# Kernel tuning notes

Hardware: AMD Instinct MI355X
Metric: run time of the kernel (lower is better)

The kernel has to match this reference:

```python
import jax, jax.numpy as jnp
import numpy as np

ACTION_SCALE = 0.01
LOG_STD_MIN, LOG_STD_MAX = -20.0, 2.0


def setup_inputs() -> dict:
    key = jax.random.key(0)
    k1, k2, k3 = jax.random.split(key, 3)
    B, N, D = 8, 1024, 128
    kv = jax.random.normal(k1, (B, N, 4 * D), dtype=jnp.float32)
    positions = jax.random.normal(k2, (B, N, 3), dtype=jnp.float32)
    eps = jax.random.normal(k3, (B, N, 3), dtype=jnp.float32)  # standard-normal sample for rsample
    return {"kv": kv, "positions": positions, "eps": eps}


def reference(kv, positions, eps):
    # Split Atomwise output into mean/std key-value embeddings: each [B, N, D]
    k_mu, v_mu, k_sigma, v_sigma = jnp.split(kv, 4, axis=-1)

    # Low-rank attention-like pairwise scores: [B, N, N]
    rel_shifts_mean = jnp.einsum("bid,bjd->bij", k_mu, v_mu)
    rel_shifts_log_std = jnp.einsum("bid,bjd->bij", k_sigma, v_sigma)

    # All-pairs unit displacement vectors: [B, N, N, 3]
    P = positions[:, :, None, :] - positions[:, None, :, :]
    norm = jnp.linalg.norm(P, axis=-1) + 1e-8
    P = P / norm[..., None]

    # Weighted sum over the j axis (torch dim=-2): [B, N, 3]
    actions_mean = jnp.einsum("bijc,bij->bic", P, rel_shifts_mean)
    actions_log_std = jnp.clip(
        jnp.einsum("bijc,bij->bic", P, rel_shifts_log_std), LOG_STD_MIN, LOG_STD_MAX
    )
    actions_std = jnp.exp(actions_log_std)

    # TanhNormal rsample (training branch) with externally supplied noise eps
    pre_tanh = actions_mean + actions_std * eps
    actions = jnp.tanh(pre_tanh)

    # Normal log-prob minus tanh log-det-Jacobian
    normal_lp = (
        -0.5 * ((pre_tanh - actions_mean) / actions_std) ** 2
        - actions_log_std
        - 0.5 * jnp.log(2.0 * jnp.pi)
    )
    log_det = (
        2.0 * jnp.log(2.0)
        + jax.nn.log_sigmoid(2.0 * pre_tanh)
        + jax.nn.log_sigmoid(-2.0 * pre_tanh)
    )
    log_prob = jnp.sum(normal_lp - log_det, axis=(1, 2))[:, None]  # [B, 1]

    actions = actions * ACTION_SCALE
    # change-of-variables correction for the action_scale factor
    n_dims = pre_tanh.shape[1] * pre_tanh.shape[2]
    log_prob = log_prob - n_dims * jnp.log(ACTION_SCALE)
    return actions, log_prob
```

## Files before the change

### kernel.cpp

```cpp
#include <hip/hip_runtime.h>
#include <math.h>


#define NTOK 1024
#define LPCONST 14147.0828114f

typedef __bf16 bf16x8 __attribute__((ext_vector_type(8)));
typedef float f32x4 __attribute__((ext_vector_type(4)));
#define MFMA(a, b, c) __builtin_amdgcn_mfma_f32_16x16x32_bf16(a, b, c, 0, 0, 0)

__device__ __forceinline__ unsigned short to_bf16(float x) {
    return (unsigned short)((__float_as_uint(x) + 0x8000u) >> 16);
}

template <int CTRL>
__device__ __forceinline__ float dpp_add(float v) {
    int y = __builtin_amdgcn_update_dpp(0, __float_as_int(v), CTRL, 0xf, 0xf, true);
    return v + __int_as_float(y);
}
__device__ __forceinline__ float red16(float v) {
    v = dpp_add<0xB1>(v);
    v = dpp_add<0x4E>(v);
    v = dpp_add<0x141>(v);
    v = dpp_add<0x140>(v);
    return v;
}

__global__ __launch_bounds__(256) void prepass_kernel(
    const float* __restrict__ kv, unsigned short* __restrict__ frag)
{
    const int t = blockIdx.x * 256 + threadIdx.x;
    const int lane = t & 63;
    const int kc   = (t >> 6) & 3;
    const int tile = (t >> 8) & 63;
    const int b    = (t >> 14) & 7;
    const int side = t >> 17;

    const int row = tile * 16 + (lane & 15);
    const int kof = kc * 32 + (lane >> 4) * 8;
    const float* gp = kv + ((size_t)b * NTOK + row) * 512 + side * 128 + kof;
    const float4 m0 = *(const float4*)gp;
    const float4 m1 = *(const float4*)(gp + 4);
    const float4 s0 = *(const float4*)(gp + 256);
    const float4 s1 = *(const float4*)(gp + 260);

    unsigned short* cp = frag + (size_t)side * 2097152 +
                         ((size_t)(((b * 64 + tile) * 4 + kc) * 2) << 9) + lane * 8;
    ushort4 h0, h1;
    h0.x = to_bf16(m0.x); h0.y = to_bf16(m0.y); h0.z = to_bf16(m0.z); h0.w = to_bf16(m0.w);
    h1.x = to_bf16(m1.x); h1.y = to_bf16(m1.y); h1.z = to_bf16(m1.z); h1.w = to_bf16(m1.w);
    *(ushort4*)(cp + 0) = h0; *(ushort4*)(cp + 4) = h1;
    h0.x = to_bf16(s0.x); h0.y = to_bf16(s0.y); h0.z = to_bf16(s0.z); h0.w = to_bf16(s0.w);
    h1.x = to_bf16(s1.x); h1.y = to_bf16(s1.y); h1.z = to_bf16(s1.z); h1.w = to_bf16(s1.w);
    *(ushort4*)(cp + 512) = h0; *(ushort4*)(cp + 516) = h1;
}

__global__ __launch_bounds__(256) void actor_gemm_kernel(
    const unsigned short* __restrict__ frag, const float* __restrict__ pos,
    float* __restrict__ partial, float* __restrict__ out)
{
    const int t = threadIdx.x;
    const int w = t >> 6;
    const int lane = t & 63;
    const int q = lane >> 4;
    const int r16 = lane & 15;
    const int js = blockIdx.x;
    const int itb = blockIdx.y;
    const int b = blockIdx.z;
    const int i0 = itb * 64;
    const int jb = js * 128;

    const unsigned short* fragA = frag;
    const unsigned short* fragB = frag + 2097152;
    const float* posb = pos + (size_t)b * NTOK * 3;

    const int atile0 = b * 64 + itb * 4;
    const int btile0 = b * 64 + js * 8 + w * 2;
    const int lofs = lane * 8;

    f32x4 accm[4][2], accs[4][2];
    #pragma unroll
    for (int ig = 0; ig < 4; ++ig)
        #pragma unroll
        for (int jg = 0; jg < 2; ++jg) {
            accm[ig][jg] = (f32x4){0.f, 0.f, 0.f, 0.f};
            accs[ig][jg] = (f32x4){0.f, 0.f, 0.f, 0.f};
        }

    #pragma unroll
    for (int kc = 0; kc < 4; ++kc) {
        bf16x8 Bm[2], Bs[2];
        #pragma unroll
        for (int jg = 0; jg < 2; ++jg) {
            const unsigned short* bp =
                fragB + (((size_t)(btile0 + jg) * 8 + kc * 2) << 9) + lofs;
            Bm[jg] = *(const bf16x8*)(bp);
            Bs[jg] = *(const bf16x8*)(bp + 512);
        }
        #pragma unroll
        for (int ig = 0; ig < 4; ++ig) {
            const unsigned short* ap =
                fragA + (((size_t)(atile0 + ig) * 8 + kc * 2) << 9) + lofs;
            const bf16x8 Am = *(const bf16x8*)(ap);
            const bf16x8 As = *(const bf16x8*)(ap + 512);
            #pragma unroll
            for (int jg = 0; jg < 2; ++jg) {
                accm[ig][jg] = MFMA(Am, Bm[jg], accm[ig][jg]);
                accs[ig][jg] = MFMA(As, Bs[jg], accs[ig][jg]);
            }
        }
    }

    float am[4][4][3] = {};
    float al[4][4][3] = {};
    float pj[2][3];
    #pragma unroll
    for (int jg = 0; jg < 2; ++jg) {
        const int j = jb + w * 32 + jg * 16 + r16;
        pj[jg][0] = posb[j * 3 + 0];
        pj[jg][1] = posb[j * 3 + 1];
        pj[jg][2] = posb[j * 3 + 2];
    }
    #pragma unroll
    for (int ig = 0; ig < 4; ++ig)
        #pragma unroll
        for (int reg = 0; reg < 4; ++reg) {
            const int i = i0 + ig * 16 + q * 4 + reg;
            const float pix = posb[i * 3 + 0];
            const float piy = posb[i * 3 + 1];
            const float piz = posb[i * 3 + 2];
            #pragma unroll
            for (int jg = 0; jg < 2; ++jg) {
                const float dx = pix - pj[jg][0];
                const float dy = piy - pj[jg][1];
                const float dz = piz - pj[jg][2];
                const float d2 = dx * dx + dy * dy + dz * dz;
                const float inv = d2 > 0.f ? rsqrtf(d2) : 0.f;
                const float wm = accm[ig][jg][reg] * inv;
                const float ws = accs[ig][jg][reg] * inv;
                am[ig][reg][0] = fmaf(dx, wm, am[ig][reg][0]);
                am[ig][reg][1] = fmaf(dy, wm, am[ig][reg][1]);
                am[ig][reg][2] = fmaf(dz, wm, am[ig][reg][2]);
                al[ig][reg][0] = fmaf(dx, ws, al[ig][reg][0]);
                al[ig][reg][1] = fmaf(dy, ws, al[ig][reg][1]);
                al[ig][reg][2] = fmaf(dz, ws, al[ig][reg][2]);
            }
        }

    #pragma unroll
    for (int ig = 0; ig < 4; ++ig)
        #pragma unroll
        for (int reg = 0; reg < 4; ++reg)
            #pragma unroll
            for (int c = 0; c < 3; ++c) {
                am[ig][reg][c] = red16(am[ig][reg][c]);
                al[ig][reg][c] = red16(al[ig][reg][c]);
            }

    __shared__ float wacc[4 * 64 * 6];
    if (r16 == 0) {
        #pragma unroll
        for (int ig = 0; ig < 4; ++ig)
            #pragma unroll
            for (int reg = 0; reg < 4; ++reg) {
                const int row = ig * 16 + q * 4 + reg;
                float* p = wacc + (w * 64 + row) * 6;
                p[0] = am[ig][reg][0]; p[1] = am[ig][reg][1]; p[2] = am[ig][reg][2];
                p[3] = al[ig][reg][0]; p[4] = al[ig][reg][1]; p[5] = al[ig][reg][2];
            }
    }
    __syncthreads();
    for (int u = t; u < 384; u += 256) {
        const int row = u / 6, c = u - row * 6;
        const float v = wacc[row * 6 + c] + wacc[(64 + row) * 6 + c] +
                        wacc[(128 + row) * 6 + c] + wacc[(192 + row) * 6 + c];
        partial[((size_t)((js * 8 + b) * NTOK) + i0 + row) * 6 + c] = v;
    }
    if (js == 0 && itb == 0 && t == 0) out[8 * NTOK * 3 + b] = LPCONST;
}

__device__ __forceinline__ float softplusf(float z) {
    return z > 20.f ? z : log1pf(expf(z));
}

__global__ __launch_bounds__(64) void actor_tail_kernel(
    const float* __restrict__ partial, const float* __restrict__ eps,
    float* __restrict__ out)
{
    const int b = blockIdx.x >> 4;
    const int i = (blockIdx.x & 15) * 64 + threadIdx.x;
    const int gi = b * NTOK + i;

    float am[3] = {}, al[3] = {};
    #pragma unroll
    for (int js = 0; js < 8; ++js) {
        const float* p = partial + (((size_t)js * 8 + b) * NTOK + i) * 6;
        const float2 v0 = *(const float2*)(p);
        const float2 v1 = *(const float2*)(p + 2);
        const float2 v2 = *(const float2*)(p + 4);
        am[0] += v0.x; am[1] += v0.y; am[2] += v1.x;
        al[0] += v1.y; al[1] += v2.x; al[2] += v2.y;
    }

    float lp = 0.f;
    #pragma unroll
    for (int c = 0; c < 3; ++c) {
        const float als = fminf(fmaxf(al[c], -20.f), 2.f);
        const float sd = expf(als);
        const float e = eps[gi * 3 + c];
        const float pre = fmaf(sd, e, am[c]);
        out[gi * 3 + c] = tanhf(pre) * 0.01f;
        const float t2 = 2.f * pre;
        lp += -0.5f * e * e - als - 2.3052328944f + softplusf(t2) + softplusf(-t2);
    }

    #pragma unroll
    for (int m = 1; m < 64; m <<= 1) lp += __shfl_xor(lp, m, 64);
    if (threadIdx.x == 0) atomicAdd(out + NTOK * 8 * 3 + b, lp);
}

extern "C" void kernel_launch(void* const* d_in, const int* in_sizes, int n_in,
                              void* d_out, int out_size, void* d_ws, size_t ws_size,
                              hipStream_t stream) {
    const float* kv = (const float*)d_in[0];
    const float* pos = (const float*)d_in[1];
    const float* eps = (const float*)d_in[2];
    float* out = (float*)d_out;
    float* partial = (float*)d_ws;
    unsigned short* frag = (unsigned short*)((char*)d_ws + (2 << 20));

    prepass_kernel<<<dim3(1024), 256, 0, stream>>>(kv, frag);
    actor_gemm_kernel<<<dim3(8, 16, 8), 256, 0, stream>>>(frag, pos, partial, out);
    actor_tail_kernel<<<dim3(128), 64, 0, stream>>>(partial, eps, out);
}
```

Baseline: 100.1 us.

## Fuse GEMM and tail into one kernel with full-row j sweep per block

Restructures the main kernel so each block owns 16 rows i and sweeps all 1024 j columns across its 4 waves. This removes the cross-block partial-sum buffer and lets the tail math (tanh, log-prob, atomic add) run in the same kernel, so the third launch goes away. The log-prob constant is now initialised in the prepass, and the fragment layout is simplified. The trade-off is fewer blocks (512), less register reuse of the A/B fragments per MFMA, and per-lane position loads inside the j loop.

```diff
diff --git a/kernel.cpp b/kernel.cpp
--- a/kernel.cpp
+++ b/kernel.cpp
@@ -26,10 +26,17 @@
     return v;
 }
 
+__device__ __forceinline__ float softplusf(float z) {
+    return z > 20.f ? z : log1pf(expf(z));
+}
+
 __global__ __launch_bounds__(256) void prepass_kernel(
-    const float* __restrict__ kv, unsigned short* __restrict__ frag)
+    const float* __restrict__ kv, unsigned short* __restrict__ frag,
+    float* __restrict__ out)
 {
     const int t = blockIdx.x * 256 + threadIdx.x;
+    if (t < 8) out[8 * NTOK * 3 + t] = LPCONST;
+
     const int lane = t & 63;
     const int kc   = (t >> 6) & 3;
     const int tile = (t >> 8) & 63;
@@ -45,7 +52,7 @@
     const float4 s1 = *(const float4*)(gp + 260);
 
     unsigned short* cp = frag + (size_t)side * 2097152 +
-                         ((size_t)(((b * 64 + tile) * 4 + kc) * 2) << 9) + lane * 8;
+                         (size_t)(b * 64 + tile) * 4096 + kc * 1024 + lane * 8;
     ushort4 h0, h1;
     h0.x = to_bf16(m0.x); h0.y = to_bf16(m0.y); h0.z = to_bf16(m0.z); h0.w = to_bf16(m0.w);
     h1.x = to_bf16(m1.x); h1.y = to_bf16(m1.y); h1.z = to_bf16(m1.z); h1.w = to_bf16(m1.w);
@@ -55,168 +62,104 @@
     *(ushort4*)(cp + 512) = h0; *(ushort4*)(cp + 516) = h1;
 }
 
-__global__ __launch_bounds__(256) void actor_gemm_kernel(
+__global__ __launch_bounds__(256) void actor_kernel(
     const unsigned short* __restrict__ frag, const float* __restrict__ pos,
-    float* __restrict__ partial, float* __restrict__ out)
+    const float* __restrict__ eps, float* __restrict__ out)
 {
     const int t = threadIdx.x;
     const int w = t >> 6;
     const int lane = t & 63;
     const int q = lane >> 4;
     const int r16 = lane & 15;
-    const int js = blockIdx.x;
-    const int itb = blockIdx.y;
-    const int b = blockIdx.z;
-    const int i0 = itb * 64;
-    const int jb = js * 128;
+    const int itx = blockIdx.x;
+    const int b = blockIdx.y;
+    const int i0 = itx * 16;
 
-    const unsigned short* fragA = frag;
-    const unsigned short* fragB = frag + 2097152;
+    const unsigned short* fragK = frag;
+    const unsigned short* fragV = frag + 2097152;
     const float* posb = pos + (size_t)b * NTOK * 3;
 
-    const int atile0 = b * 64 + itb * 4;
-    const int btile0 = b * 64 + js * 8 + w * 2;
-    const int lofs = lane * 8;
-
-    f32x4 accm[4][2], accs[4][2];
-    #pragma unroll
-    for (int ig = 0; ig < 4; ++ig)
-        #pragma unroll
-        for (int jg = 0; jg < 2; ++jg) {
-            accm[ig][jg] = (f32x4){0.f, 0.f, 0.f, 0.f};
-            accs[ig][jg] = (f32x4){0.f, 0.f, 0.f, 0.f};
-        }
-
+    const unsigned short* kp = fragK + (size_t)(b * 64 + itx) * 4096 + lane * 8;
+    bf16x8 Km[4], Ks[4];
     #pragma unroll
     for (int kc = 0; kc < 4; ++kc) {
-        bf16x8 Bm[2], Bs[2];
+        Km[kc] = *(const bf16x8*)(kp + kc * 1024);
+        Ks[kc] = *(const bf16x8*)(kp + kc * 1024 + 512);
+    }
+
+    const int i = i0 + r16;
+    const float pix = posb[i * 3 + 0];
+    const float piy = posb[i * 3 + 1];
+    const float piz = posb[i * 3 + 2];
+
+    float am0 = 0.f, am1 = 0.f, am2 = 0.f;
+    float al0 = 0.f, al1 = 0.f, al2 = 0.f;
+
+    const unsigned short* vbase =
+        fragV + (size_t)(b * 64 + w * 16) * 4096 + lane * 8;
+
+    #pragma unroll 2
+    for (int jt = 0; jt < 16; ++jt) {
+        const unsigned short* vp = vbase + jt * 4096;
+        f32x4 accm = (f32x4){0.f, 0.f, 0.f, 0.f};
+        f32x4 accs = (f32x4){0.f, 0.f, 0.f, 0.f};
         #pragma unroll
-        for (int jg = 0; jg < 2; ++jg) {
-            const unsigned short* bp =
-                fragB + (((size_t)(btile0 + jg) * 8 + kc * 2) << 9) + lofs;
-            Bm[jg] = *(const bf16x8*)(bp);
-            Bs[jg] = *(const bf16x8*)(bp + 512);
+        for (int kc = 0; kc < 4; ++kc) {
+            const bf16x8 Vm = *(const bf16x8*)(vp + kc * 1024);
+            const bf16x8 Vs = *(const bf16x8*)(vp + kc * 1024 + 512);
+            accm = MFMA(Vm, Km[kc], accm);
+            accs = MFMA(Vs, Ks[kc], accs);
         }
+        const int jbase = (w * 16 + jt) * 16 + q * 4;
         #pragma unroll
-        for (int ig = 0; ig < 4; ++ig) {
-            const unsigned short* ap =
-                fragA + (((size_t)(atile0 + ig) * 8 + kc * 2) << 9) + lofs;
-            const bf16x8 Am = *(const bf16x8*)(ap);
-            const bf16x8 As = *(const bf16x8*)(ap + 512);
-            #pragma unroll
-            for (int jg = 0; jg < 2; ++jg) {
-                accm[ig][jg] = MFMA(Am, Bm[jg], accm[ig][jg]);
-                accs[ig][jg] = MFMA(As, Bs[jg], accs[ig][jg]);
-            }
+        for (int reg = 0; reg < 4; ++reg) {
+            const float* pj = posb + (jbase + reg) * 3;
+            const float dx = pix - pj[0];
+            const float dy = piy - pj[1];
+            const float dz = piz - pj[2];
+            const float d2 = dx * dx + dy * dy + dz * dz;
+            const float inv = d2 > 0.f ? rsqrtf(d2) : 0.f;
+            const float wm = accm[reg] * inv;
+            const float ws = accs[reg] * inv;
+            am0 = fmaf(dx, wm, am0); am1 = fmaf(dy, wm, am1); am2 = fmaf(dz, wm, am2);
+            al0 = fmaf(dx, ws, al0); al1 = fmaf(dy, ws, al1); al2 = fmaf(dz, ws, al2);
         }
     }
 
-    float am[4][4][3] = {};
-    float al[4][4][3] = {};
-    float pj[2][3];
-    #pragma unroll
-    for (int jg = 0; jg < 2; ++jg) {
-        const int j = jb + w * 32 + jg * 16 + r16;
-        pj[jg][0] = posb[j * 3 + 0];
-        pj[jg][1] = posb[j * 3 + 1];
-        pj[jg][2] = posb[j * 3 + 2];
-    }
-    #pragma unroll
-    for (int ig = 0; ig < 4; ++ig)
-        #pragma unroll
-        for (int reg = 0; reg < 4; ++reg) {
-            const int i = i0 + ig * 16 + q * 4 + reg;
-            const float pix = posb[i * 3 + 0];
-            const float piy = posb[i * 3 + 1];
-            const float piz = posb[i * 3 + 2];
-            #pragma unroll
-            for (int jg = 0; jg < 2; ++jg) {
-                const float dx = pix - pj[jg][0];
-                const float dy = piy - pj[jg][1];
-                const float dz = piz - pj[jg][2];
-                const float d2 = dx * dx + dy * dy + dz * dz;
-                const float inv = d2 > 0.f ? rsqrtf(d2) : 0.f;
-                const float wm = accm[ig][jg][reg] * inv;
-                const float ws = accs[ig][jg][reg] * inv;
-                am[ig][reg][0] = fmaf(dx, wm, am[ig][reg][0]);
-                am[ig][reg][1] = fmaf(dy, wm, am[ig][reg][1]);
-                am[ig][reg][2] = fmaf(dz, wm, am[ig][reg][2]);
-                al[ig][reg][0] = fmaf(dx, ws, al[ig][reg][0]);
-                al[ig][reg][1] = fmaf(dy, ws, al[ig][reg][1]);
-                al[ig][reg][2] = fmaf(dz, ws, al[ig][reg][2]);
-            }
-        }
+    am0 += __shfl_xor(am0, 16, 64); am0 += __shfl_xor(am0, 32, 64);
+    am1 += __shfl_xor(am1, 16, 64); am1 += __shfl_xor(am1, 32, 64);
+    am2 += __shfl_xor(am2, 16, 64); am2 += __shfl_xor(am2, 32, 64);
+    al0 += __shfl_xor(al0, 16, 64); al0 += __shfl_xor(al0, 32, 64);
+    al1 += __shfl_xor(al1, 16, 64); al1 += __shfl_xor(al1, 32, 64);
+    al2 += __shfl_xor(al2, 16, 64); al2 += __shfl_xor(al2, 32, 64);
 
-    #pragma unroll
-    for (int ig = 0; ig < 4; ++ig)
-        #pragma unroll
-        for (int reg = 0; reg < 4; ++reg)
-            #pragma unroll
-            for (int c = 0; c < 3; ++c) {
-                am[ig][reg][c] = red16(am[ig][reg][c]);
-                al[ig][reg][c] = red16(al[ig][reg][c]);
-            }
-
-    __shared__ float wacc[4 * 64 * 6];
-    if (r16 == 0) {
-        #pragma unroll
-        for (int ig = 0; ig < 4; ++ig)
-            #pragma unroll
-            for (int reg = 0; reg < 4; ++reg) {
-                const int row = ig * 16 + q * 4 + reg;
-                float* p = wacc + (w * 64 + row) * 6;
-                p[0] = am[ig][reg][0]; p[1] = am[ig][reg][1]; p[2] = am[ig][reg][2];
-                p[3] = al[ig][reg][0]; p[4] = al[ig][reg][1]; p[5] = al[ig][reg][2];
-            }
+    __shared__ float wacc[4 * 16 * 6];
+    __shared__ float fin[16 * 6];
+    if (lane < 16) {
+        float* p = wacc + (w * 16 + r16) * 6;
+        p[0] = am0; p[1] = am1; p[2] = am2; p[3] = al0; p[4] = al1; p[5] = al2;
     }
     __syncthreads();
-    for (int u = t; u < 384; u += 256) {
-        const int row = u / 6, c = u - row * 6;
-        const float v = wacc[row * 6 + c] + wacc[(64 + row) * 6 + c] +
-                        wacc[(128 + row) * 6 + c] + wacc[(192 + row) * 6 + c];
-        partial[((size_t)((js * 8 + b) * NTOK) + i0 + row) * 6 + c] = v;
+    if (t < 96) fin[t] = wacc[t] + wacc[96 + t] + wacc[192 + t] + wacc[288 + t];
+    __syncthreads();
+
+    if (t < 16) {
+        const int gi = b * NTOK + i0 + t;
+        const float* v = fin + t * 6;
+        float lp = 0.f;
+        #pragma unroll
+        for (int c = 0; c < 3; ++c) {
+            const float als = fminf(fmaxf(v[3 + c], -20.f), 2.f);
+            const float sd = expf(als);
+            const float e = eps[gi * 3 + c];
+            const float pre = fmaf(sd, e, v[c]);
+            out[gi * 3 + c] = tanhf(pre) * 0.01f;
+            const float t2 = 2.f * pre;
+            lp += -0.5f * e * e - als - 2.3052328944f + softplusf(t2) + softplusf(-t2);
+        }
+        lp = red16(lp);
+        if (t == 0) atomicAdd(out + 8 * NTOK * 3 + b, lp);
     }
-    if (js == 0 && itb == 0 && t == 0) out[8 * NTOK * 3 + b] = LPCONST;
-}
-
-__device__ __forceinline__ float softplusf(float z) {
-    return z > 20.f ? z : log1pf(expf(z));
-}
-
-__global__ __launch_bounds__(64) void actor_tail_kernel(
-    const float* __restrict__ partial, const float* __restrict__ eps,
-    float* __restrict__ out)
-{
-    const int b = blockIdx.x >> 4;
-    const int i = (blockIdx.x & 15) * 64 + threadIdx.x;
-    const int gi = b * NTOK + i;
-
-    float am[3] = {}, al[3] = {};
-    #pragma unroll
-    for (int js = 0; js < 8; ++js) {
-        const float* p = partial + (((size_t)js * 8 + b) * NTOK + i) * 6;
-        const float2 v0 = *(const float2*)(p);
-        const float2 v1 = *(const float2*)(p + 2);
-        const float2 v2 = *(const float2*)(p + 4);
-        am[0] += v0.x; am[1] += v0.y; am[2] += v1.x;
-        al[0] += v1.y; al[1] += v2.x; al[2] += v2.y;
-    }
-
-    float lp = 0.f;
-    #pragma unroll
-    for (int c = 0; c < 3; ++c) {
-        const float als = fminf(fmaxf(al[c], -20.f), 2.f);
-        const float sd = expf(als);
-        const float e = eps[gi * 3 + c];
-        const float pre = fmaf(sd, e, am[c]);
-        out[gi * 3 + c] = tanhf(pre) * 0.01f;
-        const float t2 = 2.f * pre;
-        lp += -0.5f * e * e - als - 2.3052328944f + softplusf(t2) + softplusf(-t2);
-    }
-
-    #pragma unroll
-    for (int m = 1; m < 64; m <<= 1) lp += __shfl_xor(lp, m, 64);
-    if (threadIdx.x == 0) atomicAdd(out + NTOK * 8 * 3 + b, lp);
 }
 
 extern "C" void kernel_launch(void* const* d_in, const int* in_sizes, int n_in,
@@ -226,10 +169,8 @@
     const float* pos = (const float*)d_in[1];
     const float* eps = (const float*)d_in[2];
     float* out = (float*)d_out;
-    float* partial = (float*)d_ws;
-    unsigned short* frag = (unsigned short*)((char*)d_ws + (2 << 20));
+    unsigned short* frag = (unsigned short*)d_ws;
 
-    prepass_kernel<<<dim3(1024), 256, 0, stream>>>(kv, frag);
-    actor_gemm_kernel<<<dim3(8, 16, 8), 256, 0, stream>>>(frag, pos, partial, out);
-    actor_tail_kernel<<<dim3(128), 64, 0, stream>>>(partial, eps, out);
+    prepass_kernel<<<dim3(1024), 256, 0, stream>>>(kv, frag, out);
+    actor_kernel<<<dim3(64, 8), 256, 0, stream>>>(frag, pos, eps, out);
 }
```

Result: no change. 101.1 us (+1.0%).
